# Kernel tuning notes

Measured on AMD Instinct MI355X. Metric: run time of the kernel, lower is better.

The kernel has to match this reference:

```python
import jax, jax.numpy as jnp
import numpy as np

B, M, N = 2097152, 6, 3
SQUARINGS = 8   # fixed scaling: ||T||_F <~ sqrt(M) ~ 2.5, so ||A|| ~ 0.01 after scaling
ORDER = 12     # Taylor order; gives ~machine precision at this scaled norm


def _expm(T):
    """Batched matrix exponential via fixed scaling-and-squaring + Horner Taylor.
    T: [B, N, N]. Numerically matches torch.matrix_exp for these well-scaled inputs."""
    A = T / (2.0 ** SQUARINGS)
    I = jnp.eye(T.shape[-1], dtype=T.dtype)
    # Horner: exp(A) ~ I + A(I + A/2(I + ... (I + A/ORDER)))
    E = I + A / ORDER
    for k in range(ORDER - 1, 0, -1):
        E = I + jnp.matmul(A / k, E)
    for _ in range(SQUARINGS):
        E = jnp.matmul(E, E)
    return E


def setup_inputs() -> dict:
    key = jax.random.key(0)
    kx, kc, kp = jax.random.split(key, 3)
    x = jax.random.normal(kx, (B, N, 1), dtype=jnp.float32)
    c = jax.random.normal(kc, (B, M), dtype=jnp.float32)
    psi = jax.random.normal(kp, (M, N, N), dtype=jnp.float32) * 0.1
    # per-dictionary-element Frobenius normalization, as in __init__
    psi = psi / jnp.linalg.norm(psi.reshape(M, -1), axis=1)[:, None, None]
    return {"x": x, "c": c, "psi": psi}


def reference(x, c, psi):
    # T[b] = sum_m c[b,m] * psi[m]  -> [B, N, N]
    T = jnp.einsum('bm,mij->bij', c, psi)
    return jnp.matmul(_expm(T), x)  # [B, N, 1]
```

## Files before the change

kernel.cpp:

```cpp
#include <hip/hip_runtime.h>

__global__ __launch_bounds__(256) void expm_kernel(
    const float* __restrict__ x,
    const float* __restrict__ c,
    const float* __restrict__ psi,
    float* __restrict__ out)
{
    const int b = blockIdx.x * blockDim.x + threadIdx.x;

    const float2* c2 = reinterpret_cast<const float2*>(c + (size_t)b * 6);
    const float2 ca = c2[0], cb = c2[1], cc = c2[2];
    const float cm[6] = {ca.x, ca.y, cb.x, cb.y, cc.x, cc.y};

    float T[9];
#pragma unroll
    for (int j = 0; j < 9; ++j) {
        float s = cm[0] * psi[0 * 9 + j];
#pragma unroll
        for (int m = 1; m < 6; ++m) s = fmaf(cm[m], psi[m * 9 + j], s);
        T[j] = s;
    }

    const float trT  = T[0] + T[4] + T[8];
    const float m01 = fmaf(T[0], T[4], -T[1] * T[3]);
    const float m02 = fmaf(T[0], T[8], -T[2] * T[6]);
    const float m12 = fmaf(T[4], T[8], -T[5] * T[7]);
    const float msT = m01 + m02 + m12;
    const float M10 = fmaf(T[3], T[8], -T[5] * T[6]);
    const float M20 = fmaf(T[3], T[7], -T[4] * T[6]);
    const float detT = fmaf(T[0], m12, fmaf(-T[1], M10, T[2] * M20));
    const float c2v = trT * 0.25f;
    const float c1v = msT * -0.0625f;
    const float c0v = detT * 0.015625f;

    const float d2 = fmaf(c2v, c2v, c1v);
    const float d1 = fmaf(c2v, c1v, c0v);
    const float d0 = c2v * c0v;

    float p0 = 0.0f, p1 = 0.0f, p2 = 1.0f;
    float b0 = 1.0f, b1 = 1.0f, b2 = 0.5f;
    const float invfact[9] = {0, 0, 0,
        1.6666667e-1f,
        4.1666667e-2f,
        8.3333333e-3f,
        1.3888889e-3f,
        1.9841270e-4f,
        2.4801587e-5f};
#pragma unroll
    for (int k = 3; k <= 8; ++k) {
        const float t0 = c0v * p2;
        const float t1 = fmaf(c1v, p2, p0);
        const float t2 = fmaf(c2v, p2, p1);
        p0 = t0; p1 = t1; p2 = t2;
        const float f = invfact[k];
        b0 = fmaf(p0, f, b0);
        b1 = fmaf(p1, f, b1);
        b2 = fmaf(p2, f, b2);
    }

#pragma unroll
    for (int s2 = 0; s2 < 2; ++s2) {
        const float q0 = b0 * b0;
        const float q1 = 2.0f * (b0 * b1);
        const float q2 = fmaf(b1, b1, 2.0f * (b0 * b2));
        const float q3 = 2.0f * (b1 * b2);
        const float q4 = b2 * b2;
        b0 = fmaf(d0, q4, fmaf(c0v, q3, q0));
        b1 = fmaf(d1, q4, fmaf(c1v, q3, q1));
        b2 = fmaf(d2, q4, fmaf(c2v, q3, q2));
    }
    const float b1q = b1 * 0.25f;
    const float b2q = b2 * 0.0625f;

    const float* xb = x + (size_t)b * 3;
    const float x0 = xb[0], x1 = xb[1], x2 = xb[2];
    const float w0 = fmaf(T[0], x0, fmaf(T[1], x1, T[2] * x2));
    const float w1 = fmaf(T[3], x0, fmaf(T[4], x1, T[5] * x2));
    const float w2 = fmaf(T[6], x0, fmaf(T[7], x1, T[8] * x2));
    const float v0 = fmaf(T[0], w0, fmaf(T[1], w1, T[2] * w2));
    const float v1 = fmaf(T[3], w0, fmaf(T[4], w1, T[5] * w2));
    const float v2 = fmaf(T[6], w0, fmaf(T[7], w1, T[8] * w2));

    float* ob = out + (size_t)b * 3;
    ob[0] = fmaf(b0, x0, fmaf(b1q, w0, b2q * v0));
    ob[1] = fmaf(b0, x1, fmaf(b1q, w1, b2q * v1));
    ob[2] = fmaf(b0, x2, fmaf(b1q, w2, b2q * v2));
}

extern "C" void kernel_launch(void* const* d_in, const int* in_sizes, int n_in,
                              void* d_out, int out_size, void* d_ws, size_t ws_size,
                              hipStream_t stream) {
    const float* x   = (const float*)d_in[0];
    const float* c   = (const float*)d_in[1];
    const float* psi = (const float*)d_in[2];
    float* out = (float*)d_out;

    const int B = in_sizes[1] / 6;
    const int block = 256;
    const int grid = B / block;
    expm_kernel<<<grid, block, 0, stream>>>(x, c, psi, out);
}
```

Baseline: 103.4 us.

## Process two batch elements per thread with wider loads and constant-memory psi

Each thread now handles two matrices, loading c as three float4s and x and out as three float2s each, so global accesses are wider and more regular. psi is copied into __constant__ memory with an async device-to-device memcpy before the launch, so all threads read it through the constant path. This halves the thread count and doubles per-thread register work. It also adds a memcpy operation on the stream, which may land inside the timed region.

```diff
diff --git a/kernel.cpp b/kernel.cpp
--- a/kernel.cpp
+++ b/kernel.cpp
@@ -1,102 +1,118 @@
 #include <hip/hip_runtime.h>
 
+__constant__ float g_psi[54];
+
 __global__ __launch_bounds__(256) void expm_kernel(
-    const float* __restrict__ x,
-    const float* __restrict__ c,
-    const float* __restrict__ psi,
-    float* __restrict__ out)
+    const float2* __restrict__ x2,
+    const float4* __restrict__ c4,
+    float2* __restrict__ o2)
 {
-    const int b = blockIdx.x * blockDim.x + threadIdx.x;
+    const int t = blockIdx.x * blockDim.x + threadIdx.x;
 
-    const float2* c2 = reinterpret_cast<const float2*>(c + (size_t)b * 6);
-    const float2 ca = c2[0], cb = c2[1], cc = c2[2];
-    const float cm[6] = {ca.x, ca.y, cb.x, cb.y, cc.x, cc.y};
+    const float4 cA = c4[(size_t)t * 3 + 0];
+    const float4 cB = c4[(size_t)t * 3 + 1];
+    const float4 cC = c4[(size_t)t * 3 + 2];
+    const float2 xA = x2[(size_t)t * 3 + 0];
+    const float2 xB = x2[(size_t)t * 3 + 1];
+    const float2 xC = x2[(size_t)t * 3 + 2];
 
-    float T[9];
+    const float cm[2][6] = {{cA.x, cA.y, cA.z, cA.w, cB.x, cB.y},
+                            {cB.z, cB.w, cC.x, cC.y, cC.z, cC.w}};
+    const float xs[2][3] = {{xA.x, xA.y, xB.x}, {xB.y, xC.x, xC.y}};
+    float ys[2][3];
+
 #pragma unroll
-    for (int j = 0; j < 9; ++j) {
-        float s = cm[0] * psi[0 * 9 + j];
+    for (int u = 0; u < 2; ++u) {
+        float T[9];
 #pragma unroll
-        for (int m = 1; m < 6; ++m) s = fmaf(cm[m], psi[m * 9 + j], s);
-        T[j] = s;
+        for (int j = 0; j < 9; ++j) {
+            float s = cm[u][0] * g_psi[0 * 9 + j];
+#pragma unroll
+            for (int m = 1; m < 6; ++m) s = fmaf(cm[u][m], g_psi[m * 9 + j], s);
+            T[j] = s;
+        }
+
+        const float trT = T[0] + T[4] + T[8];
+        const float m01 = fmaf(T[0], T[4], -T[1] * T[3]);
+        const float m02 = fmaf(T[0], T[8], -T[2] * T[6]);
+        const float m12 = fmaf(T[4], T[8], -T[5] * T[7]);
+        const float msT = m01 + m02 + m12;
+        const float M10 = fmaf(T[3], T[8], -T[5] * T[6]);
+        const float M20 = fmaf(T[3], T[7], -T[4] * T[6]);
+        const float detT = fmaf(T[0], m12, fmaf(-T[1], M10, T[2] * M20));
+        const float c2v = trT * 0.25f;
+        const float c1v = msT * -0.0625f;
+        const float c0v = detT * 0.015625f;
+
+        const float d2 = fmaf(c2v, c2v, c1v);
+        const float d1 = fmaf(c2v, c1v, c0v);
+        const float d0 = c2v * c0v;
+
+        float p0 = 0.0f, p1 = 0.0f, p2 = 1.0f;
+        float b0 = 1.0f, b1 = 1.0f, b2 = 0.5f;
+        const float invfact[9] = {0, 0, 0,
+            1.6666667e-1f, 4.1666667e-2f, 8.3333333e-3f,
+            1.3888889e-3f, 1.9841270e-4f, 2.4801587e-5f};
+#pragma unroll
+        for (int k = 3; k <= 8; ++k) {
+            const float t0 = c0v * p2;
+            const float t1 = fmaf(c1v, p2, p0);
+            const float t2 = fmaf(c2v, p2, p1);
+            p0 = t0; p1 = t1; p2 = t2;
+            const float f = invfact[k];
+            b0 = fmaf(p0, f, b0);
+            b1 = fmaf(p1, f, b1);
+            b2 = fmaf(p2, f, b2);
+        }
+
+#pragma unroll
+        for (int s2 = 0; s2 < 2; ++s2) {
+            const float q0 = b0 * b0;
+            const float q1 = 2.0f * (b0 * b1);
+            const float q2 = fmaf(b1, b1, 2.0f * (b0 * b2));
+            const float q3 = 2.0f * (b1 * b2);
+            const float q4 = b2 * b2;
+            b0 = fmaf(d0, q4, fmaf(c0v, q3, q0));
+            b1 = fmaf(d1, q4, fmaf(c1v, q3, q1));
+            b2 = fmaf(d2, q4, fmaf(c2v, q3, q2));
+        }
+        const float b1q = b1 * 0.25f;
+        const float b2q = b2 * 0.0625f;
+
+        const float x0 = xs[u][0], x1 = xs[u][1], x2v = xs[u][2];
+        const float w0 = fmaf(T[0], x0, fmaf(T[1], x1, T[2] * x2v));
+        const float w1 = fmaf(T[3], x0, fmaf(T[4], x1, T[5] * x2v));
+        const float w2 = fmaf(T[6], x0, fmaf(T[7], x1, T[8] * x2v));
+        const float v0 = fmaf(T[0], w0, fmaf(T[1], w1, T[2] * w2));
+        const float v1 = fmaf(T[3], w0, fmaf(T[4], w1, T[5] * w2));
+        const float v2 = fmaf(T[6], w0, fmaf(T[7], w1, T[8] * w2));
+        ys[u][0] = fmaf(b0, x0, fmaf(b1q, w0, b2q * v0));
+        ys[u][1] = fmaf(b0, x1, fmaf(b1q, w1, b2q * v1));
+        ys[u][2] = fmaf(b0, x2v, fmaf(b1q, w2, b2q * v2));
     }
 
-    const float trT  = T[0] + T[4] + T[8];
-    const float m01 = fmaf(T[0], T[4], -T[1] * T[3]);
-    const float m02 = fmaf(T[0], T[8], -T[2] * T[6]);
-    const float m12 = fmaf(T[4], T[8], -T[5] * T[7]);
-    const float msT = m01 + m02 + m12;
-    const float M10 = fmaf(T[3], T[8], -T[5] * T[6]);
-    const float M20 = fmaf(T[3], T[7], -T[4] * T[6]);
-    const float detT = fmaf(T[0], m12, fmaf(-T[1], M10, T[2] * M20));
-    const float c2v = trT * 0.25f;
-    const float c1v = msT * -0.0625f;
-    const float c0v = detT * 0.015625f;
-
-    const float d2 = fmaf(c2v, c2v, c1v);
-    const float d1 = fmaf(c2v, c1v, c0v);
-    const float d0 = c2v * c0v;
-
-    float p0 = 0.0f, p1 = 0.0f, p2 = 1.0f;
-    float b0 = 1.0f, b1 = 1.0f, b2 = 0.5f;
-    const float invfact[9] = {0, 0, 0,
-        1.6666667e-1f,
-        4.1666667e-2f,
-        8.3333333e-3f,
-        1.3888889e-3f,
-        1.9841270e-4f,
-        2.4801587e-5f};
-#pragma unroll
-    for (int k = 3; k <= 8; ++k) {
-        const float t0 = c0v * p2;
-        const float t1 = fmaf(c1v, p2, p0);
-        const float t2 = fmaf(c2v, p2, p1);
-        p0 = t0; p1 = t1; p2 = t2;
-        const float f = invfact[k];
-        b0 = fmaf(p0, f, b0);
-        b1 = fmaf(p1, f, b1);
-        b2 = fmaf(p2, f, b2);
-    }
-
-#pragma unroll
-    for (int s2 = 0; s2 < 2; ++s2) {
-        const float q0 = b0 * b0;
-        const float q1 = 2.0f * (b0 * b1);
-        const float q2 = fmaf(b1, b1, 2.0f * (b0 * b2));
-        const float q3 = 2.0f * (b1 * b2);
-        const float q4 = b2 * b2;
-        b0 = fmaf(d0, q4, fmaf(c0v, q3, q0));
-        b1 = fmaf(d1, q4, fmaf(c1v, q3, q1));
-        b2 = fmaf(d2, q4, fmaf(c2v, q3, q2));
-    }
-    const float b1q = b1 * 0.25f;
-    const float b2q = b2 * 0.0625f;
-
-    const float* xb = x + (size_t)b * 3;
-    const float x0 = xb[0], x1 = xb[1], x2 = xb[2];
-    const float w0 = fmaf(T[0], x0, fmaf(T[1], x1, T[2] * x2));
-    const float w1 = fmaf(T[3], x0, fmaf(T[4], x1, T[5] * x2));
-    const float w2 = fmaf(T[6], x0, fmaf(T[7], x1, T[8] * x2));
-    const float v0 = fmaf(T[0], w0, fmaf(T[1], w1, T[2] * w2));
-    const float v1 = fmaf(T[3], w0, fmaf(T[4], w1, T[5] * w2));
-    const float v2 = fmaf(T[6], w0, fmaf(T[7], w1, T[8] * w2));
-
-    float* ob = out + (size_t)b * 3;
-    ob[0] = fmaf(b0, x0, fmaf(b1q, w0, b2q * v0));
-    ob[1] = fmaf(b0, x1, fmaf(b1q, w1, b2q * v1));
-    ob[2] = fmaf(b0, x2, fmaf(b1q, w2, b2q * v2));
+    float2 oA, oB, oC;
+    oA.x = ys[0][0]; oA.y = ys[0][1];
+    oB.x = ys[0][2]; oB.y = ys[1][0];
+    oC.x = ys[1][1]; oC.y = ys[1][2];
+    o2[(size_t)t * 3 + 0] = oA;
+    o2[(size_t)t * 3 + 1] = oB;
+    o2[(size_t)t * 3 + 2] = oC;
 }
 
 extern "C" void kernel_launch(void* const* d_in, const int* in_sizes, int n_in,
                               void* d_out, int out_size, void* d_ws, size_t ws_size,
                               hipStream_t stream) {
-    const float* x   = (const float*)d_in[0];
-    const float* c   = (const float*)d_in[1];
-    const float* psi = (const float*)d_in[2];
-    float* out = (float*)d_out;
+    const float2* x2 = (const float2*)d_in[0];
+    const float4* c4 = (const float4*)d_in[1];
+    float2* o2 = (float2*)d_out;
+
+    hipMemcpyToSymbolAsync(HIP_SYMBOL(g_psi), d_in[2], 54 * sizeof(float), 0,
+                           hipMemcpyDeviceToDevice, stream);
 
     const int B = in_sizes[1] / 6;
+    const int Tn = B / 2;
     const int block = 256;
-    const int grid = B / block;
-    expm_kernel<<<grid, block, 0, stream>>>(x, c, psi, out);
+    const int grid = Tn / block;
+    expm_kernel<<<grid, block, 0, stream>>>(x2, c4, o2);
 }
```

New measurement: 110.4 us. +6.8%, slower.
